# Kernel tuning notes

Hardware: AMD Instinct MI355X
Metric: run time of the kernel (lower is better)

Reference implementation:

```python
import jax, jax.numpy as jnp
import numpy as np

OUT, IN, G = 12288, 4096, 128       # out_features, in_features, group_size
IN_GROUPS = IN // G                 # 32
QMAX = 15                           # wbit=4


def setup_inputs() -> dict:
    key = jax.random.key(0)
    k1, k2, k3, k4, k5 = jax.random.split(key, 5)
    x = jax.random.normal(k1, (8, IN), dtype=jnp.float32)
    # packed 4-bit codes: two nibbles per byte, high nibble first
    qcodes = jax.random.randint(k2, (OUT, IN_GROUPS, G // 2), 0, 256, dtype=jnp.int32).astype(jnp.uint8)
    scales = jax.random.uniform(k3, (OUT, IN_GROUPS), dtype=jnp.float32, minval=0.005, maxval=0.02)
    zeros = jax.random.uniform(k4, (OUT, IN_GROUPS), dtype=jnp.float32, minval=0.0, maxval=float(QMAX))
    bias = jax.random.normal(k5, (OUT,), dtype=jnp.float32) * 0.01
    return {"x": x, "qcodes": qcodes, "scales": scales, "zeros": zeros, "bias": bias}


def _dequant_weight(qcodes, scales, zeros):
    # unpack nibbles: q[0::2] = high nibble, q[1::2] = low nibble (matches torch packing)
    hi = (qcodes >> 4) & 0xF                     # [OUT, IN_GROUPS, G//2]
    lo = qcodes & 0xF
    q = jnp.stack([hi, lo], axis=-1).reshape(OUT, IN_GROUPS, G).astype(jnp.float32)
    W = (q - zeros[..., None]) * scales[..., None]   # per-group affine dequant
    # torch reference casts to fp16 and slices to in_features
    return W.reshape(OUT, IN_GROUPS * G)[:, :IN].astype(jnp.float16)


def reference(x, qcodes, scales, zeros, bias):
    W = _dequant_weight(qcodes, scales, zeros)   # [OUT, IN] fp16
    return x @ W.astype(x.dtype).T + bias        # F.linear(x, W, bias)
```

## Files before the change

### kernel.cpp

```cpp
#include <hip/hip_runtime.h>
#include <cstdint>

#define OUTF 12288
#define INF  4096
#define NG   32
#define BATCH 8

#define BLOCK 512
#define WAVES 8
#define RPW 3
#define RPB (WAVES*RPW)
#define NBLK (OUTF/RPB)

typedef _Float16 half2_t __attribute__((ext_vector_type(2)));

__device__ __forceinline__ float dot2(half2_t a, half2_t b, float c) {
#if __has_builtin(__builtin_amdgcn_fdot2)
    return __builtin_amdgcn_fdot2(a, b, c, false);
#else
    return c + (float)(a.x) * (float)(b.x) + (float)(a.y) * (float)(b.y);
#endif
}

__device__ __forceinline__ half2_t pk16(float a, float b) {
    return __builtin_bit_cast(half2_t, __builtin_amdgcn_cvt_pkrtz(a, b));
}

__global__ __launch_bounds__(BLOCK, 4) void qlin_kernel(
    const float* __restrict__ x,
    const int*   __restrict__ qc,
    const float* __restrict__ scales,
    const float* __restrict__ zeros,
    const float* __restrict__ bias,
    float* __restrict__ out)
{
    __shared__ uint4 xs[4096];

    const int tid  = threadIdx.x;
    const int wave = tid >> 6;
    const int lane = tid & 63;
    const int row0 = blockIdx.x * RPB + wave * RPW;

    #pragma unroll
    for (int i = 0; i < 8; ++i) {
        const float4 v0 = *reinterpret_cast<const float4*>(x + i * INF + tid * 8);
        const float4 v1 = *reinterpret_cast<const float4*>(x + i * INF + tid * 8 + 4);
        uint4 w;
        w.x = __builtin_bit_cast(uint32_t, pk16(v0.x, v0.y));
        w.y = __builtin_bit_cast(uint32_t, pk16(v0.z, v0.w));
        w.z = __builtin_bit_cast(uint32_t, pk16(v1.x, v1.y));
        w.w = __builtin_bit_cast(uint32_t, pk16(v1.z, v1.w));
        xs[i * 512 + tid] = w;
    }

    const int* qp[RPW];
    const float* scb[RPW];
    const float* zpb[RPW];
    #pragma unroll
    for (int r = 0; r < RPW; ++r) {
        const int o = row0 + r;
        qp[r]  = qc + o * 2048 + lane * 4;
        scb[r] = scales + o * NG + (lane >> 4);
        zpb[r] = zeros  + o * NG + (lane >> 4);
    }

    uint4 tA[RPW], tB[RPW];
    float sA[RPW], nzA[RPW], sB[RPW], nzB[RPW];
    #pragma unroll
    for (int r = 0; r < RPW; ++r) {
        tA[r]  = *reinterpret_cast<const uint4*>(qp[r]);
        tB[r]  = *reinterpret_cast<const uint4*>(qp[r] + 256);
        sA[r]  = scb[r][0];
        nzA[r] = -zpb[r][0] * sA[r];
    }

    float y[RPW][BATCH];
    #pragma unroll
    for (int r = 0; r < RPW; ++r)
        #pragma unroll
        for (int b = 0; b < BATCH; ++b) y[r][b] = 0.f;

    __syncthreads();

    #pragma unroll
    for (int h = 0; h < 8; ++h) {
        uint4 tN[RPW];
        if (h < 6) {
            #pragma unroll
            for (int r = 0; r < RPW; ++r)
                tN[r] = *reinterpret_cast<const uint4*>(qp[r] + (h + 2) * 256);
        }
        if (h < 7) {
            #pragma unroll
            for (int r = 0; r < RPW; ++r) {
                sB[r]  = scb[r][(h + 1) * 4];
                nzB[r] = -zpb[r][(h + 1) * 4] * sB[r];
            }
        }

        half2_t wp[RPW][4];
        #pragma unroll
        for (int r = 0; r < RPW; ++r) {
            #pragma unroll
            for (int e = 0; e < 4; ++e) {
                const uint32_t ei = (e == 0) ? tA[r].x : (e == 1) ? tA[r].y
                                 : (e == 2) ? tA[r].z : tA[r].w;
                const float hi = (float)((ei >> 4) & 0xFu);
                const float lo = (float)( ei       & 0xFu);
                wp[r][e] = pk16(fmaf(hi, sA[r], nzA[r]),
                                fmaf(lo, sA[r], nzA[r]));
            }
        }

        const int slot = h * 64 + lane;
        #pragma unroll
        for (int b = 0; b < BATCH; ++b) {
            const uint4 v = xs[b * 512 + slot];
            const half2_t x0 = __builtin_bit_cast(half2_t, v.x);
            const half2_t x1 = __builtin_bit_cast(half2_t, v.y);
            const half2_t x2 = __builtin_bit_cast(half2_t, v.z);
            const half2_t x3 = __builtin_bit_cast(half2_t, v.w);
            #pragma unroll
            for (int r = 0; r < RPW; ++r) {
                y[r][b] = dot2(wp[r][0], x0, y[r][b]);
                y[r][b] = dot2(wp[r][1], x1, y[r][b]);
                y[r][b] = dot2(wp[r][2], x2, y[r][b]);
                y[r][b] = dot2(wp[r][3], x3, y[r][b]);
            }
        }

        #pragma unroll
        for (int r = 0; r < RPW; ++r) {
            tA[r] = tB[r];
            if (h < 6) tB[r] = tN[r];
            if (h < 7) { sA[r] = sB[r]; nzA[r] = nzB[r]; }
        }
    }

    float keep = 0.f;
    #pragma unroll
    for (int r = 0; r < RPW; ++r) {
        #pragma unroll
        for (int b = 0; b < BATCH; ++b) {
            float v = y[r][b];
            #pragma unroll
            for (int m = 1; m < 64; m <<= 1) v += __shfl_xor(v, m, 64);
            if (lane == r * 8 + b) keep = v;
        }
    }
    if (lane < RPW * BATCH) {
        const int r = lane >> 3, b = lane & 7;
        const int o = row0 + r;
        out[b * OUTF + o] = keep + bias[o];
    }
}

extern "C" void kernel_launch(void* const* d_in, const int* in_sizes, int n_in,
                              void* d_out, int out_size, void* d_ws, size_t ws_size,
                              hipStream_t stream) {
    const float* x      = (const float*)d_in[0];
    const int*   qcodes = (const int*)  d_in[1];
    const float* scales = (const float*)d_in[2];
    const float* zeros  = (const float*)d_in[3];
    const float* bias   = (const float*)d_in[4];
    float* out = (float*)d_out;

    qlin_kernel<<<NBLK, BLOCK, 0, stream>>>(x, qcodes, scales, zeros, bias, out);
}
```

Before: 27.56 us.

## Split K across two blocks with fp16 pre-conversion and a combine pass

Splits the inner dimension into two halves, each handled by its own block, and launches twice as many blocks with fewer rows per wave. This is meant to raise occupancy and memory-level parallelism for the weight stream. The x-to-fp16 conversion moves into a separate small kernel, so each block stages only its half of x in shared memory. A third kernel adds the two partial sums and the bias. In exchange there are two extra launches and a round trip of the partial sums through the workspace. The old kernel remains as a fallback for when the workspace is too small.

```diff
diff --git a/kernel.cpp b/kernel.cpp
--- a/kernel.cpp
+++ b/kernel.cpp
@@ -8,9 +8,13 @@
 
 #define BLOCK 512
 #define WAVES 8
-#define RPW 3
+#define RPW 2
 #define RPB (WAVES*RPW)
-#define NBLK (OUTF/RPB)
+#define NBLK ((OUTF/RPB)*2)
+
+#define WS_X16_BYTES   65536
+#define WS_PART_FLOATS 98304
+#define WS_NEEDED      (WS_X16_BYTES + 2*WS_PART_FLOATS*4)
 
 typedef _Float16 half2_t __attribute__((ext_vector_type(2)));
 
@@ -21,26 +25,158 @@
     return c + (float)(a.x) * (float)(b.x) + (float)(a.y) * (float)(b.y);
 #endif
 }
-
 __device__ __forceinline__ half2_t pk16(float a, float b) {
     return __builtin_bit_cast(half2_t, __builtin_amdgcn_cvt_pkrtz(a, b));
 }
 
-__global__ __launch_bounds__(BLOCK, 4) void qlin_kernel(
-    const float* __restrict__ x,
-    const int*   __restrict__ qc,
-    const float* __restrict__ scales,
-    const float* __restrict__ zeros,
-    const float* __restrict__ bias,
-    float* __restrict__ out)
-{
-    __shared__ uint4 xs[4096];
+__global__ __launch_bounds__(256) void qlin_cvt(
+    const float* __restrict__ x, uint32_t* __restrict__ x16)
+{
+    const int i = blockIdx.x * 256 + threadIdx.x;
+    const float2 v = reinterpret_cast<const float2*>(x)[i];
+    x16[i] = __builtin_bit_cast(uint32_t, pk16(v.x, v.y));
+}
+
+__global__ __launch_bounds__(BLOCK, 8) void qlin_main(
+    const int*      __restrict__ qc,
+    const float*    __restrict__ scales,
+    const float*    __restrict__ zeros,
+    const uint16_t* __restrict__ x16,
+    float*          __restrict__ part)
+{
+    __shared__ uint4 xs[2048];
 
     const int tid  = threadIdx.x;
     const int wave = tid >> 6;
     const int lane = tid & 63;
-    const int row0 = blockIdx.x * RPB + wave * RPW;
-
+    const int rb   = blockIdx.x >> 1;
+    const int kh   = blockIdx.x & 1;
+    const int row0 = rb * RPB + wave * RPW;
+
+    #pragma unroll
+    for (int c = 0; c < 4; ++c) {
+        const int s = c * 64 + lane;
+        xs[wave * 256 + s] = *reinterpret_cast<const uint4*>(
+            x16 + wave * INF + kh * 2048 + s * 8);
+    }
+
+    const int* qq[RPW];
+    int soff[RPW];
+    #pragma unroll
+    for (int r = 0; r < RPW; ++r) {
+        const int o = row0 + r;
+        qq[r]   = qc + o * 2048 + kh * 1024 + lane * 4;
+        soff[r] = o * NG + kh * 16 + (lane >> 4);
+    }
+
+    uint4 tA[RPW];
+    float sA[RPW], nzA[RPW];
+    #pragma unroll
+    for (int r = 0; r < RPW; ++r) {
+        tA[r]  = *reinterpret_cast<const uint4*>(qq[r]);
+        sA[r]  = scales[soff[r]];
+        nzA[r] = -zeros[soff[r]] * sA[r];
+    }
+
+    float y[RPW][BATCH];
+    #pragma unroll
+    for (int r = 0; r < RPW; ++r)
+        #pragma unroll
+        for (int b = 0; b < BATCH; ++b) y[r][b] = 0.f;
+
+    __syncthreads();
+
+    #pragma unroll
+    for (int h = 0; h < 4; ++h) {
+        uint4 tN[RPW];
+        float sB[RPW], nzB[RPW];
+        if (h < 3) {
+            #pragma unroll
+            for (int r = 0; r < RPW; ++r) {
+                tN[r]  = *reinterpret_cast<const uint4*>(qq[r] + (h + 1) * 256);
+                sB[r]  = scales[soff[r] + (h + 1) * 4];
+                nzB[r] = -zeros[soff[r] + (h + 1) * 4] * sB[r];
+            }
+        }
+
+        half2_t wp[RPW][4];
+        #pragma unroll
+        for (int r = 0; r < RPW; ++r) {
+            #pragma unroll
+            for (int e = 0; e < 4; ++e) {
+                const uint32_t ei = (e == 0) ? tA[r].x : (e == 1) ? tA[r].y
+                                 : (e == 2) ? tA[r].z : tA[r].w;
+                const float hi = (float)((ei >> 4) & 0xFu);
+                const float lo = (float)( ei       & 0xFu);
+                wp[r][e] = pk16(fmaf(hi, sA[r], nzA[r]),
+                                fmaf(lo, sA[r], nzA[r]));
+            }
+        }
+
+        const int slot = h * 64 + lane;
+        #pragma unroll
+        for (int b = 0; b < BATCH; ++b) {
+            const uint4 v = xs[b * 256 + slot];
+            const half2_t x0 = __builtin_bit_cast(half2_t, v.x);
+            const half2_t x1 = __builtin_bit_cast(half2_t, v.y);
+            const half2_t x2 = __builtin_bit_cast(half2_t, v.z);
+            const half2_t x3 = __builtin_bit_cast(half2_t, v.w);
+            #pragma unroll
+            for (int r = 0; r < RPW; ++r) {
+                y[r][b] = dot2(wp[r][0], x0, y[r][b]);
+                y[r][b] = dot2(wp[r][1], x1, y[r][b]);
+                y[r][b] = dot2(wp[r][2], x2, y[r][b]);
+                y[r][b] = dot2(wp[r][3], x3, y[r][b]);
+            }
+        }
+
+        #pragma unroll
+        for (int r = 0; r < RPW; ++r) {
+            if (h < 3) { tA[r] = tN[r]; sA[r] = sB[r]; nzA[r] = nzB[r]; }
+        }
+    }
+
+    float keep = 0.f;
+    #pragma unroll
+    for (int r = 0; r < RPW; ++r) {
+        #pragma unroll
+        for (int b = 0; b < BATCH; ++b) {
+            float v = y[r][b];
+            #pragma unroll
+            for (int m = 1; m < 64; m <<= 1) v += __shfl_xor(v, m, 64);
+            if (lane == r * 8 + b) keep = v;
+        }
+    }
+    if (lane < RPW * BATCH) {
+        const int r = lane >> 3, b = lane & 7;
+        part[kh * WS_PART_FLOATS + b * OUTF + row0 + r] = keep;
+    }
+}
+
+__global__ __launch_bounds__(256) void qlin_combine(
+    const float* __restrict__ part, const float* __restrict__ bias,
+    float* __restrict__ out)
+{
+    const int i4 = blockIdx.x * 256 + threadIdx.x;
+    const int b  = i4 / (OUTF / 4);
+    const int o4 = (i4 - b * (OUTF / 4)) * 4;
+    const float4 p0 = *reinterpret_cast<const float4*>(part + b * OUTF + o4);
+    const float4 p1 = *reinterpret_cast<const float4*>(part + WS_PART_FLOATS + b * OUTF + o4);
+    const float4 bb = *reinterpret_cast<const float4*>(bias + o4);
+    float4 o;
+    o.x = p0.x + p1.x + bb.x; o.y = p0.y + p1.y + bb.y;
+    o.z = p0.z + p1.z + bb.z; o.w = p0.w + p1.w + bb.w;
+    *reinterpret_cast<float4*>(out + b * OUTF + o4) = o;
+}
+
+__global__ __launch_bounds__(512, 4) void qlin_fb(
+    const float* __restrict__ x, const int* __restrict__ qc,
+    const float* __restrict__ scales, const float* __restrict__ zeros,
+    const float* __restrict__ bias, float* __restrict__ out)
+{
+    __shared__ uint4 xs[4096];
+    const int tid = threadIdx.x, wave = tid >> 6, lane = tid & 63;
+    const int row0 = blockIdx.x * 24 + wave * 3;
     #pragma unroll
     for (int i = 0; i < 8; ++i) {
         const float4 v0 = *reinterpret_cast<const float4*>(x + i * INF + tid * 8);
@@ -52,103 +188,83 @@
         w.w = __builtin_bit_cast(uint32_t, pk16(v1.z, v1.w));
         xs[i * 512 + tid] = w;
     }
-
-    const int* qp[RPW];
-    const float* scb[RPW];
-    const float* zpb[RPW];
-    #pragma unroll
-    for (int r = 0; r < RPW; ++r) {
+    const int* qp[3]; const float* scb[3]; const float* zpb[3];
+    #pragma unroll
+    for (int r = 0; r < 3; ++r) {
         const int o = row0 + r;
-        qp[r]  = qc + o * 2048 + lane * 4;
+        qp[r] = qc + o * 2048 + lane * 4;
         scb[r] = scales + o * NG + (lane >> 4);
         zpb[r] = zeros  + o * NG + (lane >> 4);
     }
-
-    uint4 tA[RPW], tB[RPW];
-    float sA[RPW], nzA[RPW], sB[RPW], nzB[RPW];
-    #pragma unroll
-    for (int r = 0; r < RPW; ++r) {
-        tA[r]  = *reinterpret_cast<const uint4*>(qp[r]);
-        tB[r]  = *reinterpret_cast<const uint4*>(qp[r] + 256);
-        sA[r]  = scb[r][0];
-        nzA[r] = -zpb[r][0] * sA[r];
-    }
-
-    float y[RPW][BATCH];
-    #pragma unroll
-    for (int r = 0; r < RPW; ++r)
-        #pragma unroll
-        for (int b = 0; b < BATCH; ++b) y[r][b] = 0.f;
-
+    uint4 tA[3], tB[3]; float sA[3], nzA[3], sB[3], nzB[3];
+    #pragma unroll
+    for (int r = 0; r < 3; ++r) {
+        tA[r] = *reinterpret_cast<const uint4*>(qp[r]);
+        tB[r] = *reinterpret_cast<const uint4*>(qp[r] + 256);
+        sA[r] = scb[r][0]; nzA[r] = -zpb[r][0] * sA[r];
+    }
+    float y[3][8];
+    #pragma unroll
+    for (int r = 0; r < 3; ++r)
+        #pragma unroll
+        for (int b = 0; b < 8; ++b) y[r][b] = 0.f;
     __syncthreads();
-
     #pragma unroll
     for (int h = 0; h < 8; ++h) {
-        uint4 tN[RPW];
-        if (h < 6) {
-            #pragma unroll
-            for (int r = 0; r < RPW; ++r)
+        uint4 tN[3];
+        if (h < 6)
+            #pragma unroll
+            for (int r = 0; r < 3; ++r)
                 tN[r] = *reinterpret_cast<const uint4*>(qp[r] + (h + 2) * 256);
-        }
-        if (h < 7) {
-            #pragma unroll
-            for (int r = 0; r < RPW; ++r) {
-                sB[r]  = scb[r][(h + 1) * 4];
-                nzB[r] = -zpb[r][(h + 1) * 4] * sB[r];
-            }
-        }
-
-        half2_t wp[RPW][4];
-        #pragma unroll
-        for (int r = 0; r < RPW; ++r) {
+        if (h < 7)
+            #pragma unroll
+            for (int r = 0; r < 3; ++r) {
+                sB[r] = scb[r][(h + 1) * 4]; nzB[r] = -zpb[r][(h + 1) * 4] * sB[r];
+            }
+        half2_t wp[3][4];
+        #pragma unroll
+        for (int r = 0; r < 3; ++r)
             #pragma unroll
             for (int e = 0; e < 4; ++e) {
                 const uint32_t ei = (e == 0) ? tA[r].x : (e == 1) ? tA[r].y
                                  : (e == 2) ? tA[r].z : tA[r].w;
-                const float hi = (float)((ei >> 4) & 0xFu);
-                const float lo = (float)( ei       & 0xFu);
-                wp[r][e] = pk16(fmaf(hi, sA[r], nzA[r]),
-                                fmaf(lo, sA[r], nzA[r]));
-            }
-        }
-
+                wp[r][e] = pk16(fmaf((float)((ei >> 4) & 0xFu), sA[r], nzA[r]),
+                                fmaf((float)( ei       & 0xFu), sA[r], nzA[r]));
+            }
         const int slot = h * 64 + lane;
         #pragma unroll
-        for (int b = 0; b < BATCH; ++b) {
+        for (int b = 0; b < 8; ++b) {
             const uint4 v = xs[b * 512 + slot];
             const half2_t x0 = __builtin_bit_cast(half2_t, v.x);
             const half2_t x1 = __builtin_bit_cast(half2_t, v.y);
             const half2_t x2 = __builtin_bit_cast(half2_t, v.z);
             const half2_t x3 = __builtin_bit_cast(half2_t, v.w);
             #pragma unroll
-            for (int r = 0; r < RPW; ++r) {
+            for (int r = 0; r < 3; ++r) {
                 y[r][b] = dot2(wp[r][0], x0, y[r][b]);
                 y[r][b] = dot2(wp[r][1], x1, y[r][b]);
                 y[r][b] = dot2(wp[r][2], x2, y[r][b]);
                 y[r][b] = dot2(wp[r][3], x3, y[r][b]);
             }
         }
-
-        #pragma unroll
-        for (int r = 0; r < RPW; ++r) {
+        #pragma unroll
+        for (int r = 0; r < 3; ++r) {
             tA[r] = tB[r];
             if (h < 6) tB[r] = tN[r];
             if (h < 7) { sA[r] = sB[r]; nzA[r] = nzB[r]; }
         }
     }
-
     float keep = 0.f;
     #pragma unroll
-    for (int r = 0; r < RPW; ++r) {
-        #pragma unroll
-        for (int b = 0; b < BATCH; ++b) {
+    for (int r = 0; r < 3; ++r)
+        #pragma unroll
+        for (int b = 0; b < 8; ++b) {
             float v = y[r][b];
             #pragma unroll
             for (int m = 1; m < 64; m <<= 1) v += __shfl_xor(v, m, 64);
             if (lane == r * 8 + b) keep = v;
         }
-    }
-    if (lane < RPW * BATCH) {
+    if (lane < 24) {
         const int r = lane >> 3, b = lane & 7;
         const int o = row0 + r;
         out[b * OUTF + o] = keep + bias[o];
@@ -165,5 +281,14 @@
     const float* bias   = (const float*)d_in[4];
     float* out = (float*)d_out;
 
-    qlin_kernel<<<NBLK, BLOCK, 0, stream>>>(x, qcodes, scales, zeros, bias, out);
-}
+    if (ws_size >= (size_t)WS_NEEDED) {
+        uint32_t* x16u = (uint32_t*)d_ws;
+        float*    part = (float*)((char*)d_ws + WS_X16_BYTES);
+        qlin_cvt<<<64, 256, 0, stream>>>(x, x16u);
+        qlin_main<<<NBLK, BLOCK, 0, stream>>>(qcodes, scales, zeros,
+                                              (const uint16_t*)x16u, part);
+        qlin_combine<<<96, 256, 0, stream>>>(part, bias, out);
+    } else {
+        qlin_fb<<<512, 512, 0, stream>>>(x, qcodes, scales, zeros, bias, out);
+    }
+}
```

Measured after the change: 38.73 us. 40.5% more time.

## Stream packed weight codes through LDS ring via direct global-to-LDS loads

Applied to the files above, without the earlier changes.

Replaces the register double-buffered global loads of packed 4-bit codes with direct global-to-LDS loads into a per-wave two-slot ring, gated by manual vmcnt waits. Scales and zeros for the block's rows are staged once into shared memory, and the launch-bounds occupancy hint drops from 4 to 2. The aim is to free vector registers and overlap weight streaming with dequant/dot compute. It adds LDS usage and relies on hand-counted waitcnt ordering, which interacts fragilely with the x staging loads issued afterward.

```diff
diff --git a/kernel.cpp b/kernel.cpp
--- a/kernel.cpp
+++ b/kernel.cpp
@@ -21,12 +21,17 @@
     return c + (float)(a.x) * (float)(b.x) + (float)(a.y) * (float)(b.y);
 #endif
 }
-
 __device__ __forceinline__ half2_t pk16(float a, float b) {
     return __builtin_bit_cast(half2_t, __builtin_amdgcn_cvt_pkrtz(a, b));
 }
 
-__global__ __launch_bounds__(BLOCK, 4) void qlin_kernel(
+__device__ __forceinline__ void gload_lds16(const int* g, void* l) {
+    __builtin_amdgcn_global_load_lds(
+        (const __attribute__((address_space(1))) uint32_t*)g,
+        (__attribute__((address_space(3))) uint32_t*)l, 16, 0, 0);
+}
+
+__global__ __launch_bounds__(BLOCK, 2) void qlin_kernel(
     const float* __restrict__ x,
     const int*   __restrict__ qc,
     const float* __restrict__ scales,
@@ -35,11 +40,26 @@
     float* __restrict__ out)
 {
     __shared__ uint4 xs[4096];
+    __shared__ uint4 qring[WAVES * 2 * RPW * 64];
+    __shared__ float scz[RPB * NG * 2];
 
-    const int tid  = threadIdx.x;
-    const int wave = tid >> 6;
-    const int lane = tid & 63;
-    const int row0 = blockIdx.x * RPB + wave * RPW;
+    const int tid   = threadIdx.x;
+    const int wave  = tid >> 6;
+    const int lane  = tid & 63;
+    const int rbase = blockIdx.x * RPB;
+    const int row0  = rbase + wave * RPW;
+
+    const int* qq[RPW];
+    #pragma unroll
+    for (int r = 0; r < RPW; ++r)
+        qq[r] = qc + (row0 + r) * 2048 + lane * 4;
+
+    #pragma unroll
+    for (int r = 0; r < RPW; ++r)
+        gload_lds16(qq[r],       &qring[((wave * 2 + 0) * RPW + r) * 64]);
+    #pragma unroll
+    for (int r = 0; r < RPW; ++r)
+        gload_lds16(qq[r] + 256, &qring[((wave * 2 + 1) * RPW + r) * 64]);
 
     #pragma unroll
     for (int i = 0; i < 8; ++i) {
@@ -53,25 +73,10 @@
         xs[i * 512 + tid] = w;
     }
 
-    const int* qp[RPW];
-    const float* scb[RPW];
-    const float* zpb[RPW];
-    #pragma unroll
-    for (int r = 0; r < RPW; ++r) {
-        const int o = row0 + r;
-        qp[r]  = qc + o * 2048 + lane * 4;
-        scb[r] = scales + o * NG + (lane >> 4);
-        zpb[r] = zeros  + o * NG + (lane >> 4);
-    }
-
-    uint4 tA[RPW], tB[RPW];
-    float sA[RPW], nzA[RPW], sB[RPW], nzB[RPW];
-    #pragma unroll
-    for (int r = 0; r < RPW; ++r) {
-        tA[r]  = *reinterpret_cast<const uint4*>(qp[r]);
-        tB[r]  = *reinterpret_cast<const uint4*>(qp[r] + 256);
-        sA[r]  = scb[r][0];
-        nzA[r] = -zpb[r][0] * sA[r];
+    for (int i = tid; i < RPB * NG; i += BLOCK) {
+        const int r = i >> 5, g = i & 31;
+        scz[i * 2]     = scales[(rbase + r) * NG + g];
+        scz[i * 2 + 1] = zeros [(rbase + r) * NG + g];
     }
 
     float y[RPW][BATCH];
@@ -84,18 +89,28 @@
 
     #pragma unroll
     for (int h = 0; h < 8; ++h) {
-        uint4 tN[RPW];
+        if (h < 7) asm volatile("s_waitcnt vmcnt(3)" ::: "memory");
+        else       asm volatile("s_waitcnt vmcnt(0)" ::: "memory");
+        __builtin_amdgcn_sched_barrier(0);
+
+        uint4 t[RPW];
+        #pragma unroll
+        for (int r = 0; r < RPW; ++r)
+            t[r] = qring[((wave * 2 + (h & 1)) * RPW + r) * 64 + lane];
+
         if (h < 6) {
             #pragma unroll
             for (int r = 0; r < RPW; ++r)
-                tN[r] = *reinterpret_cast<const uint4*>(qp[r] + (h + 2) * 256);
+                gload_lds16(qq[r] + (h + 2) * 256,
+                            &qring[((wave * 2 + (h & 1)) * RPW + r) * 64]);
         }
-        if (h < 7) {
-            #pragma unroll
-            for (int r = 0; r < RPW; ++r) {
-                sB[r]  = scb[r][(h + 1) * 4];
-                nzB[r] = -zpb[r][(h + 1) * 4] * sB[r];
-            }
+
+        float sc_[RPW], nz_[RPW];
+        #pragma unroll
+        for (int r = 0; r < RPW; ++r) {
+            const int idx = ((wave * RPW + r) * NG + (h * 4 + (lane >> 4))) * 2;
+            sc_[r] = scz[idx];
+            nz_[r] = -scz[idx + 1] * sc_[r];
         }
 
         half2_t wp[RPW][4];
@@ -103,12 +118,12 @@
         for (int r = 0; r < RPW; ++r) {
             #pragma unroll
             for (int e = 0; e < 4; ++e) {
-                const uint32_t ei = (e == 0) ? tA[r].x : (e == 1) ? tA[r].y
-                                 : (e == 2) ? tA[r].z : tA[r].w;
+                const uint32_t ei = (e == 0) ? t[r].x : (e == 1) ? t[r].y
+                                 : (e == 2) ? t[r].z : t[r].w;
                 const float hi = (float)((ei >> 4) & 0xFu);
                 const float lo = (float)( ei       & 0xFu);
-                wp[r][e] = pk16(fmaf(hi, sA[r], nzA[r]),
-                                fmaf(lo, sA[r], nzA[r]));
+                wp[r][e] = pk16(fmaf(hi, sc_[r], nz_[r]),
+                                fmaf(lo, sc_[r], nz_[r]));
             }
         }
 
@@ -127,13 +142,6 @@
                 y[r][b] = dot2(wp[r][2], x2, y[r][b]);
                 y[r][b] = dot2(wp[r][3], x3, y[r][b]);
             }
-        }
-
-        #pragma unroll
-        for (int r = 0; r < RPW; ++r) {
-            tA[r] = tB[r];
-            if (h < 6) tB[r] = tN[r];
-            if (h < 7) { sA[r] = sB[r]; nzA[r] = nzB[r]; }
         }
     }
 
```

Result: slower. 31.73 us (+15.2%).

## Use bf16 MFMA with split-K atomics and a prep kernel for activations

Applied to the files above, without the earlier changes.

Adds a prep kernel that converts x to bf16 in workspace, pads the batch to 16 rows, precomputes per-group sums of x, and initialises the output with the bias. The main kernel builds bf16 weights directly from the 4-bit codes with a bit trick (0x4300|q gives 128+q) and runs 16x16x32 bf16 MFMAs. It applies scale and zero per group afterwards using the precomputed x sums, splits K four ways and merges the partial sums with atomicAdd. This replaces the scalar dot2 dequant path with matrix cores, at the cost of a second launch, atomic contention, wasted MFMA work on the padded batch rows, and bf16 instead of fp16 precision for x. The old kernel remains as a fallback when the workspace is too small.

```diff
diff --git a/kernel.cpp b/kernel.cpp
--- a/kernel.cpp
+++ b/kernel.cpp
@@ -5,14 +5,144 @@
 #define INF  4096
 #define NG   32
 #define BATCH 8
-
-#define BLOCK 512
-#define WAVES 8
-#define RPW 3
-#define RPB (WAVES*RPW)
-#define NBLK (OUTF/RPB)
-
+#define KS   4
+
+#define WS_X16_BYTES 131072
+#define WS_SUMX_OFF  131072
+#define WS_NEEDED    (131072 + 2048)
+
+typedef short short8 __attribute__((ext_vector_type(8)));
+typedef float f32x4  __attribute__((ext_vector_type(4)));
 typedef _Float16 half2_t __attribute__((ext_vector_type(2)));
+
+__device__ __forceinline__ uint32_t cvt_pk_bf16(float lo, float hi) {
+    uint32_t r;
+    asm("v_cvt_pk_bf16_f32 %0, %1, %2" : "=v"(r) : "v"(lo), "v"(hi));
+    return r;
+}
+__device__ __forceinline__ float bf16lo_f(uint32_t w) {
+    return __builtin_bit_cast(float, w << 16);
+}
+__device__ __forceinline__ float bf16hi_f(uint32_t w) {
+    return __builtin_bit_cast(float, w & 0xFFFF0000u);
+}
+__device__ __forceinline__ uint32_t bpair(uint32_t e) {
+    return 0x43004300u | ((e >> 4) & 0xFu) | ((e & 0xFu) << 16);
+}
+
+__global__ __launch_bounds__(256) void qlin_prep(
+    const float* __restrict__ x, const float* __restrict__ bias,
+    uint32_t* __restrict__ x16, float* __restrict__ sumxT,
+    float* __restrict__ out)
+{
+    const int blk = blockIdx.x, t = threadIdx.x;
+    if (blk < 8) {
+        const float* xr = x + blk * INF + t * 16;
+        const float4 a = *reinterpret_cast<const float4*>(xr);
+        const float4 b = *reinterpret_cast<const float4*>(xr + 4);
+        const float4 c = *reinterpret_cast<const float4*>(xr + 8);
+        const float4 d = *reinterpret_cast<const float4*>(xr + 12);
+        uint32_t w[8];
+        w[0] = cvt_pk_bf16(a.x, a.y); w[1] = cvt_pk_bf16(a.z, a.w);
+        w[2] = cvt_pk_bf16(b.x, b.y); w[3] = cvt_pk_bf16(b.z, b.w);
+        w[4] = cvt_pk_bf16(c.x, c.y); w[5] = cvt_pk_bf16(c.z, c.w);
+        w[6] = cvt_pk_bf16(d.x, d.y); w[7] = cvt_pk_bf16(d.z, d.w);
+        uint4 s0 = {w[0], w[1], w[2], w[3]};
+        uint4 s1 = {w[4], w[5], w[6], w[7]};
+        reinterpret_cast<uint4*>(x16 + blk * 2048 + t * 8)[0] = s0;
+        reinterpret_cast<uint4*>(x16 + blk * 2048 + t * 8 + 4)[1 - 1] = s1;
+        float s = 0.f;
+        #pragma unroll
+        for (int i = 0; i < 8; ++i) s += bf16lo_f(w[i]) + bf16hi_f(w[i]);
+        s += __shfl_xor(s, 1, 64);
+        s += __shfl_xor(s, 2, 64);
+        s += __shfl_xor(s, 4, 64);
+        if ((t & 7) == 0) sumxT[(t >> 3) * 16 + blk] = s;
+    } else if (blk < 16) {
+        uint4 z = {0u, 0u, 0u, 0u};
+        uint4* p = reinterpret_cast<uint4*>(x16 + blk * 2048 + t * 8);
+        p[0] = z; p[1] = z;
+        if (blk == 8) {
+            const int g = t >> 3, m = 8 + (t & 7);
+            sumxT[g * 16 + m] = 0.f;
+        }
+    } else {
+        const int bb = (blk - 16) / 12;
+        const int j  = ((blk - 16) % 12) * 256 + t;
+        const float4 bv = *reinterpret_cast<const float4*>(bias + j * 4);
+        *reinterpret_cast<float4*>(out + bb * OUTF + j * 4) = bv;
+    }
+}
+
+__global__ __launch_bounds__(256, 4) void qlin_main(
+    const int*      __restrict__ qc,
+    const float*    __restrict__ scales,
+    const float*    __restrict__ zeros,
+    const uint16_t* __restrict__ x16,
+    const float*    __restrict__ sumxT,
+    float*          __restrict__ out)
+{
+    const int wid  = threadIdx.x >> 6;
+    const int lane = threadIdx.x & 63;
+    const int W    = blockIdx.x * 4 + wid;
+    const int ot   = W >> 2;
+    const int ks   = W & 3;
+    const int n16  = lane & 15;
+    const int q4   = lane >> 4;
+
+    const int ocol = (ot << 4) + n16;
+    const int* qrow = qc + ocol * 2048 + ks * 512 + q4 * 4;
+    const uint16_t* xrow = x16 + n16 * INF + ks * 1024 + q4 * 8;
+
+    const float4 sc0 = *reinterpret_cast<const float4*>(scales + ocol * NG + ks * 8);
+    const float4 sc1 = *reinterpret_cast<const float4*>(scales + ocol * NG + ks * 8 + 4);
+    const float4 zp0 = *reinterpret_cast<const float4*>(zeros  + ocol * NG + ks * 8);
+    const float4 zp1 = *reinterpret_cast<const float4*>(zeros  + ocol * NG + ks * 8 + 4);
+    const float scA[8] = {sc0.x, sc0.y, sc0.z, sc0.w, sc1.x, sc1.y, sc1.z, sc1.w};
+    const float zpA[8] = {zp0.x, zp0.y, zp0.z, zp0.w, zp1.x, zp1.y, zp1.z, zp1.w};
+
+    float y0 = 0.f, y1 = 0.f, y2 = 0.f, y3 = 0.f;
+
+    #pragma unroll
+    for (int s = 0; s < 8; ++s) {
+        const int g = ks * 8 + s;
+        uint4 qv[4], av[4];
+        #pragma unroll
+        for (int kb = 0; kb < 4; ++kb) {
+            qv[kb] = *reinterpret_cast<const uint4*>(qrow + s * 64 + kb * 16);
+            av[kb] = *reinterpret_cast<const uint4*>(xrow + s * 128 + kb * 32);
+        }
+        const float4 sx = *reinterpret_cast<const float4*>(sumxT + g * 16 + q4 * 4);
+
+        f32x4 Cg = {0.f, 0.f, 0.f, 0.f};
+        #pragma unroll
+        for (int kb = 0; kb < 4; ++kb) {
+            uint4 bw;
+            bw.x = bpair(qv[kb].x);
+            bw.y = bpair(qv[kb].y);
+            bw.z = bpair(qv[kb].z);
+            bw.w = bpair(qv[kb].w);
+            const short8 Af = __builtin_bit_cast(short8, av[kb]);
+            const short8 Bf = __builtin_bit_cast(short8, bw);
+            Cg = __builtin_amdgcn_mfma_f32_16x16x32_bf16(Af, Bf, Cg, 0, 0, 0);
+        }
+
+        const float sc = scA[s];
+        const float c1 = -sc * (128.0f + zpA[s]);
+        y0 = fmaf(sc, Cg[0], y0); y0 = fmaf(c1, sx.x, y0);
+        y1 = fmaf(sc, Cg[1], y1); y1 = fmaf(c1, sx.y, y1);
+        y2 = fmaf(sc, Cg[2], y2); y2 = fmaf(c1, sx.z, y2);
+        y3 = fmaf(sc, Cg[3], y3); y3 = fmaf(c1, sx.w, y3);
+    }
+
+    if (q4 < 2) {
+        float* op = out + (q4 * 4) * OUTF + ocol;
+        atomicAdd(op,            y0);
+        atomicAdd(op + OUTF,     y1);
+        atomicAdd(op + 2 * OUTF, y2);
+        atomicAdd(op + 3 * OUTF, y3);
+    }
+}
 
 __device__ __forceinline__ float dot2(half2_t a, half2_t b, float c) {
 #if __has_builtin(__builtin_amdgcn_fdot2)
@@ -21,26 +151,18 @@
     return c + (float)(a.x) * (float)(b.x) + (float)(a.y) * (float)(b.y);
 #endif
 }
-
 __device__ __forceinline__ half2_t pk16(float a, float b) {
     return __builtin_bit_cast(half2_t, __builtin_amdgcn_cvt_pkrtz(a, b));
 }
 
-__global__ __launch_bounds__(BLOCK, 4) void qlin_kernel(
-    const float* __restrict__ x,
-    const int*   __restrict__ qc,
-    const float* __restrict__ scales,
-    const float* __restrict__ zeros,
-    const float* __restrict__ bias,
-    float* __restrict__ out)
+__global__ __launch_bounds__(512, 4) void qlin_fb(
+    const float* __restrict__ x, const int* __restrict__ qc,
+    const float* __restrict__ scales, const float* __restrict__ zeros,
+    const float* __restrict__ bias, float* __restrict__ out)
 {
     __shared__ uint4 xs[4096];
-
-    const int tid  = threadIdx.x;
-    const int wave = tid >> 6;
-    const int lane = tid & 63;
-    const int row0 = blockIdx.x * RPB + wave * RPW;
-
+    const int tid = threadIdx.x, wave = tid >> 6, lane = tid & 63;
+    const int row0 = blockIdx.x * 24 + wave * 3;
     #pragma unroll
     for (int i = 0; i < 8; ++i) {
         const float4 v0 = *reinterpret_cast<const float4*>(x + i * INF + tid * 8);
@@ -52,103 +174,83 @@
         w.w = __builtin_bit_cast(uint32_t, pk16(v1.z, v1.w));
         xs[i * 512 + tid] = w;
     }
-
-    const int* qp[RPW];
-    const float* scb[RPW];
-    const float* zpb[RPW];
-    #pragma unroll
-    for (int r = 0; r < RPW; ++r) {
+    const int* qp[3]; const float* scb[3]; const float* zpb[3];
+    #pragma unroll
+    for (int r = 0; r < 3; ++r) {
         const int o = row0 + r;
-        qp[r]  = qc + o * 2048 + lane * 4;
+        qp[r] = qc + o * 2048 + lane * 4;
         scb[r] = scales + o * NG + (lane >> 4);
         zpb[r] = zeros  + o * NG + (lane >> 4);
     }
-
-    uint4 tA[RPW], tB[RPW];
-    float sA[RPW], nzA[RPW], sB[RPW], nzB[RPW];
-    #pragma unroll
-    for (int r = 0; r < RPW; ++r) {
-        tA[r]  = *reinterpret_cast<const uint4*>(qp[r]);
-        tB[r]  = *reinterpret_cast<const uint4*>(qp[r] + 256);
-        sA[r]  = scb[r][0];
-        nzA[r] = -zpb[r][0] * sA[r];
-    }
-
-    float y[RPW][BATCH];
-    #pragma unroll
-    for (int r = 0; r < RPW; ++r)
-        #pragma unroll
-        for (int b = 0; b < BATCH; ++b) y[r][b] = 0.f;
-
+    uint4 tA[3], tB[3]; float sA[3], nzA[3], sB[3], nzB[3];
+    #pragma unroll
+    for (int r = 0; r < 3; ++r) {
+        tA[r] = *reinterpret_cast<const uint4*>(qp[r]);
+        tB[r] = *reinterpret_cast<const uint4*>(qp[r] + 256);
+        sA[r] = scb[r][0]; nzA[r] = -zpb[r][0] * sA[r];
+    }
+    float y[3][8];
+    #pragma unroll
+    for (int r = 0; r < 3; ++r)
+        #pragma unroll
+        for (int b = 0; b < 8; ++b) y[r][b] = 0.f;
     __syncthreads();
-
     #pragma unroll
     for (int h = 0; h < 8; ++h) {
-        uint4 tN[RPW];
-        if (h < 6) {
-            #pragma unroll
-            for (int r = 0; r < RPW; ++r)
+        uint4 tN[3];
+        if (h < 6)
+            #pragma unroll
+            for (int r = 0; r < 3; ++r)
                 tN[r] = *reinterpret_cast<const uint4*>(qp[r] + (h + 2) * 256);
-        }
-        if (h < 7) {
-            #pragma unroll
-            for (int r = 0; r < RPW; ++r) {
-                sB[r]  = scb[r][(h + 1) * 4];
-                nzB[r] = -zpb[r][(h + 1) * 4] * sB[r];
+        if (h < 7)
+            #pragma unroll
+            for (int r = 0; r < 3; ++r) {
+                sB[r] = scb[r][(h + 1) * 4]; nzB[r] = -zpb[r][(h + 1) * 4] * sB[r];
             }
-        }
-
-        half2_t wp[RPW][4];
-        #pragma unroll
-        for (int r = 0; r < RPW; ++r) {
+        half2_t wp[3][4];
+        #pragma unroll
+        for (int r = 0; r < 3; ++r)
             #pragma unroll
             for (int e = 0; e < 4; ++e) {
                 const uint32_t ei = (e == 0) ? tA[r].x : (e == 1) ? tA[r].y
                                  : (e == 2) ? tA[r].z : tA[r].w;
-                const float hi = (float)((ei >> 4) & 0xFu);
-                const float lo = (float)( ei       & 0xFu);
-                wp[r][e] = pk16(fmaf(hi, sA[r], nzA[r]),
-                                fmaf(lo, sA[r], nzA[r]));
+                wp[r][e] = pk16(fmaf((float)((ei >> 4) & 0xFu), sA[r], nzA[r]),
+                                fmaf((float)( ei       & 0xFu), sA[r], nzA[r]));
             }
-        }
-
         const int slot = h * 64 + lane;
         #pragma unroll
-        for (int b = 0; b < BATCH; ++b) {
+        for (int b = 0; b < 8; ++b) {
             const uint4 v = xs[b * 512 + slot];
             const half2_t x0 = __builtin_bit_cast(half2_t, v.x);
             const half2_t x1 = __builtin_bit_cast(half2_t, v.y);
             const half2_t x2 = __builtin_bit_cast(half2_t, v.z);
             const half2_t x3 = __builtin_bit_cast(half2_t, v.w);
             #pragma unroll
-            for (int r = 0; r < RPW; ++r) {
+            for (int r = 0; r < 3; ++r) {
                 y[r][b] = dot2(wp[r][0], x0, y[r][b]);
                 y[r][b] = dot2(wp[r][1], x1, y[r][b]);
                 y[r][b] = dot2(wp[r][2], x2, y[r][b]);
                 y[r][b] = dot2(wp[r][3], x3, y[r][b]);
             }
         }
-
-        #pragma unroll
-        for (int r = 0; r < RPW; ++r) {
+        #pragma unroll
+        for (int r = 0; r < 3; ++r) {
             tA[r] = tB[r];
             if (h < 6) tB[r] = tN[r];
             if (h < 7) { sA[r] = sB[r]; nzA[r] = nzB[r]; }
         }
     }
-
     float keep = 0.f;
     #pragma unroll
-    for (int r = 0; r < RPW; ++r) {
-        #pragma unroll
-        for (int b = 0; b < BATCH; ++b) {
+    for (int r = 0; r < 3; ++r)
+        #pragma unroll
+        for (int b = 0; b < 8; ++b) {
             float v = y[r][b];
             #pragma unroll
             for (int m = 1; m < 64; m <<= 1) v += __shfl_xor(v, m, 64);
             if (lane == r * 8 + b) keep = v;
         }
-    }
-    if (lane < RPW * BATCH) {
+    if (lane < 24) {
         const int r = lane >> 3, b = lane & 7;
         const int o = row0 + r;
         out[b * OUTF + o] = keep + bias[o];
@@ -165,5 +267,13 @@
     const float* bias   = (const float*)d_in[4];
     float* out = (float*)d_out;
 
-    qlin_kernel<<<NBLK, BLOCK, 0, stream>>>(x, qcodes, scales, zeros, bias, out);
-}
+    if (ws_size >= (size_t)WS_NEEDED) {
+        uint32_t* x16  = (uint32_t*)d_ws;
+        float*    sumxT = (float*)((char*)d_ws + WS_SUMX_OFF);
+        qlin_prep<<<112, 256, 0, stream>>>(x, bias, x16, sumxT, out);
+        qlin_main<<<768, 256, 0, stream>>>(qcodes, scales, zeros,
+                                           (const uint16_t*)x16, sumxT, out);
+    } else {
+        qlin_fb<<<512, 512, 0, stream>>>(x, qcodes, scales, zeros, bias, out);
+    }
+}
```

Result: slower. 34.94 us (+26.8%).
